# Kernel tuning notes

Hardware: AMD Instinct MI355X
Metric: run time of the kernel (lower is better)

The kernel has to match this reference:

```python
import jax, jax.numpy as jnp
import numpy as np

V, B, T, D, H, HS, L, F = 50257, 16, 256, 64, 4, 16, 4, 256
EPS = 1e-5


def layernorm(x, g, b):
    mu = jnp.mean(x, axis=-1, keepdims=True)
    var = jnp.var(x, axis=-1, keepdims=True)
    return (x - mu) * jax.lax.rsqrt(var + EPS) * g + b


def setup_inputs() -> dict:
    key = jax.random.key(0)
    ks = jax.random.split(key, 20)
    s = 0.02
    inp = {
        "idx": jax.random.randint(ks[0], (B, T), 0, V),
        "targets": jax.random.randint(ks[1], (B, T), 0, V),
        "tok_emb": jax.random.normal(ks[2], (V, D), jnp.float32) * s,
        "pos_emb": jax.random.normal(ks[3], (T, D), jnp.float32) * s,
        "Wq": jax.random.normal(ks[4], (L, H, D, HS), jnp.float32) * s,
        "Wk": jax.random.normal(ks[5], (L, H, D, HS), jnp.float32) * s,
        "Wv": jax.random.normal(ks[6], (L, H, D, HS), jnp.float32) * s,
        "Wo": jax.random.normal(ks[7], (L, D, D), jnp.float32) * s,
        "bo": jnp.zeros((L, D), jnp.float32),
        "ln1_g": jnp.ones((L, D), jnp.float32),
        "ln1_b": jnp.zeros((L, D), jnp.float32),
        "ln2_g": jnp.ones((L, D), jnp.float32),
        "ln2_b": jnp.zeros((L, D), jnp.float32),
        "W1": jax.random.normal(ks[8], (L, D, F), jnp.float32) * s,
        "b1": jnp.zeros((L, F), jnp.float32),
        "W2": jax.random.normal(ks[9], (L, F, D), jnp.float32) * s,
        "b2": jnp.zeros((L, D), jnp.float32),
        "lnf_g": jnp.ones((D,), jnp.float32),
        "lnf_b": jnp.zeros((D,), jnp.float32),
        "Whead": jax.random.normal(ks[10], (D, V), jnp.float32) * s,
        "bhead": jnp.zeros((V,), jnp.float32),
    }
    return inp


def reference(idx, targets, tok_emb, pos_emb, Wq, Wk, Wv, Wo, bo,
              ln1_g, ln1_b, ln2_g, ln2_b, W1, b1, W2, b2,
              lnf_g, lnf_b, Whead, bhead):
    Tt = idx.shape[1]
    x = tok_emb[idx] + pos_emb[:Tt]  # [B,T,D]
    causal = jnp.tril(jnp.ones((Tt, Tt), bool))
    for l in range(L):
        h = layernorm(x, ln1_g[l], ln1_b[l])
        q = jnp.einsum('btd,hds->bhts', h, Wq[l])
        k = jnp.einsum('btd,hds->bhts', h, Wk[l])
        v = jnp.einsum('btd,hds->bhts', h, Wv[l])
        # NOTE: original applies NO 1/sqrt(head_size) scaling
        scores = jnp.einsum('bhts,bhus->bhtu', q, k)  # [B,H,T,T]
        scores = jnp.where(causal, scores, -jnp.inf)
        attn = jax.nn.softmax(scores, axis=-1)
        o = jnp.einsum('bhtu,bhus->bths', attn, v)  # [B,T,H,HS]
        o = o.reshape(o.shape[0], Tt, D)
        x = x + o @ Wo[l] + bo[l]
        h2 = layernorm(x, ln2_g[l], ln2_b[l])
        x = x + jax.nn.relu(h2 @ W1[l] + b1[l]) @ W2[l] + b2[l]
    x = layernorm(x, lnf_g, lnf_b)
    logits = x @ Whead + bhead  # [B,T,V]
    logp = jax.nn.log_softmax(logits, axis=-1)
    loss = -jnp.mean(jnp.take_along_axis(logp, targets[..., None], axis=-1))
    return (logits, loss)
```

## Files before the change

### kernel.cpp

```cpp
#include <hip/hip_runtime.h>
#include <hip/hip_bf16.h>
#include <math.h>

constexpr int NV  = 50257;
constexpr int NB  = 16;
constexpr int NT  = 256;
constexpr int ND  = 64;
constexpr int NH  = 4;
constexpr int NHS = 16;
constexpr int NL  = 4;
constexpr int NF  = 256;
constexpr int NN  = NB * NT;
constexpr float EPS = 1e-5f;

constexpr int NCB2 = 200;
constexpr int NVP  = NCB2 * 256;
constexpr int LOGITS = NN * NV;
constexpr int RB_N  = NN / 64;
constexpr int CB_PER_XCD = NCB2 / 8;

constexpr int X_OFF   = 0;
constexpr int Q_OFF   = X_OFF  + NN * ND;
constexpr int K_OFF   = Q_OFF  + NN * ND;
constexpr int V_OFF   = K_OFF  + NN * ND;
constexpr int O_OFF   = V_OFF  + NN * ND;
constexpr int A_OFF   = O_OFF  + NN * ND;
constexpr int XFB_OFF = A_OFF  + NN * NF;
constexpr int WM_OFF  = XFB_OFF + NN * ND / 2;
constexpr int WS2_OFF = WM_OFF + NCB2 * NN;
constexpr int WHB_OFF = WS2_OFF + NCB2 * NN;
constexpr int LP_OFF  = WHB_OFF + NVP * 32;

typedef __bf16 bf16x8 __attribute__((ext_vector_type(8)));
typedef float  f32x4  __attribute__((ext_vector_type(4)));

__global__ __launch_bounds__(256) void k_ln_qkv(
        float* __restrict__ x, const float* __restrict__ g, const float* __restrict__ bb,
        const float* __restrict__ Wq, const float* __restrict__ Wk, const float* __restrict__ Wv,
        float* __restrict__ q, float* __restrict__ k, float* __restrict__ v,
        const int* __restrict__ idx, const float* __restrict__ tok,
        const float* __restrict__ pos, int first) {
    __shared__ float hs[16][65];
    int t = threadIdx.x;
    int r0 = blockIdx.x * 16;
    if (first) {
        for (int i = t; i < 16 * 64; i += 256) {
            int n = r0 + (i >> 6);
            int tt = n & (NT - 1), d = i & 63;
            float e = tok[idx[n] * ND + d] + pos[tt * ND + d];
            hs[i >> 6][i & 63] = e;
            x[(size_t)r0 * 64 + i] = e;
        }
    } else {
        for (int i = t; i < 16 * 64; i += 256)
            hs[i >> 6][i & 63] = x[r0 * 64 + i];
    }
    __syncthreads();
    {
        int row = t >> 4, sub = t & 15;
        float s = 0.f, s2 = 0.f;
        #pragma unroll
        for (int j = 0; j < 4; j++) { float vv = hs[row][sub * 4 + j]; s += vv; s2 += vv * vv; }
        #pragma unroll
        for (int off = 1; off < 16; off <<= 1) { s += __shfl_xor(s, off); s2 += __shfl_xor(s2, off); }
        float mu = s * (1.f / 64.f);
        float var = s2 * (1.f / 64.f) - mu * mu;
        float rs = rsqrtf(var + EPS);
        #pragma unroll
        for (int j = 0; j < 4; j++) {
            int d = sub * 4 + j;
            hs[row][d] = (hs[row][d] - mu) * rs * g[d] + bb[d];
        }
    }
    __syncthreads();
    int c = t & 63, rg = t >> 6;
    int head = c >> 4, sidx = c & 15;
    float aq[4], ak[4], av[4];
    #pragma unroll
    for (int i = 0; i < 4; i++) { aq[i] = 0.f; ak[i] = 0.f; av[i] = 0.f; }
    for (int kk = 0; kk < 64; kk++) {
        float wq = Wq[(head * 64 + kk) * 16 + sidx];
        float wk = Wk[(head * 64 + kk) * 16 + sidx];
        float wv = Wv[(head * 64 + kk) * 16 + sidx];
        #pragma unroll
        for (int i = 0; i < 4; i++) {
            float h = hs[rg * 4 + i][kk];
            aq[i] += h * wq; ak[i] += h * wk; av[i] += h * wv;
        }
    }
    #pragma unroll
    for (int i = 0; i < 4; i++) {
        int n = r0 + rg * 4 + i;
        int b = n >> 8, tt = n & 255;
        int oidx = ((b * NH + head) * NT + tt) * NHS + sidx;
        q[oidx] = aq[i]; k[oidx] = ak[i]; v[oidx] = av[i];
    }
}

__global__ __launch_bounds__(256) void k_attn(
        const float* __restrict__ q, const float* __restrict__ k,
        const float* __restrict__ v, float* __restrict__ o) {
    __shared__ float ks[256][16];
    __shared__ float vs[256][16];
    int blk = blockIdx.x;
    int bh = blk >> 2;
    int tq = blk & 3;
    int t = threadIdx.x;
    int tl = t >> 2, sub = t & 3;
    int tt = tq * 64 + tl;
    int nrows = tq * 64 + 64;
    const float* kb = k + bh * NT * NHS;
    const float* vb = v + bh * NT * NHS;
    for (int i = t; i < nrows * 16; i += 256) {
        (&ks[0][0])[i] = kb[i];
        (&vs[0][0])[i] = vb[i];
    }
    __syncthreads();
    float qr[16];
    const float* qp = q + bh * NT * NHS + tt * NHS;
    #pragma unroll
    for (int j = 0; j < 16; j += 4) {
        float4 qv = *(const float4*)(qp + j);
        qr[j] = qv.x; qr[j+1] = qv.y; qr[j+2] = qv.z; qr[j+3] = qv.w;
    }
    float m = -1e30f, l = 0.f, acc[16];
    #pragma unroll
    for (int j = 0; j < 16; j++) acc[j] = 0.f;
    for (int u = sub; u <= tt; u += 4) {
        float s = 0.f;
        #pragma unroll
        for (int j = 0; j < 16; j++) s += qr[j] * ks[u][j];
        float mn = fmaxf(m, s);
        float corr = __expf(m - mn);
        float p = __expf(s - mn);
        l = l * corr + p;
        #pragma unroll
        for (int j = 0; j < 16; j++) acc[j] = acc[j] * corr + p * vs[u][j];
        m = mn;
    }
    #pragma unroll
    for (int off = 1; off < 4; off <<= 1) {
        float mo = __shfl_xor(m, off);
        float lo = __shfl_xor(l, off);
        float mn = fmaxf(m, mo);
        float c1 = __expf(m - mn), c2 = __expf(mo - mn);
        l = l * c1 + lo * c2;
        #pragma unroll
        for (int j = 0; j < 16; j++) {
            float ao = __shfl_xor(acc[j], off);
            acc[j] = acc[j] * c1 + ao * c2;
        }
        m = mn;
    }
    float inv = 1.f / l;
    int b = bh >> 2, h = bh & 3;
    float* op = o + (b * NT + tt) * ND + h * NHS;
    float o0, o1, o2, o3;
    if (sub == 0)      { o0 = acc[0];  o1 = acc[1];  o2 = acc[2];  o3 = acc[3];  }
    else if (sub == 1) { o0 = acc[4];  o1 = acc[5];  o2 = acc[6];  o3 = acc[7];  }
    else if (sub == 2) { o0 = acc[8];  o1 = acc[9];  o2 = acc[10]; o3 = acc[11]; }
    else               { o0 = acc[12]; o1 = acc[13]; o2 = acc[14]; o3 = acc[15]; }
    float4 ov = make_float4(o0 * inv, o1 * inv, o2 * inv, o3 * inv);
    *(float4*)(op + sub * 4) = ov;
}

__global__ __launch_bounds__(256) void k_post(
        const float* __restrict__ o, const float* __restrict__ Wo, const float* __restrict__ bo,
        const float* __restrict__ g2, const float* __restrict__ bg2,
        const float* __restrict__ W1, const float* __restrict__ b1,
        const float* __restrict__ W2, const float* __restrict__ b2m,
        float* __restrict__ x,
        const float* __restrict__ lg, const float* __restrict__ lb,
        __hip_bfloat16* __restrict__ xfb, int last) {
    __shared__ float os[16][65];
    __shared__ float xs[16][65];
    __shared__ float as[16][257];
    int t = threadIdx.x;
    int r0 = blockIdx.x * 16;
    for (int i = t; i < 16 * 64; i += 256)
        os[i >> 6][i & 63] = o[r0 * 64 + i];
    __syncthreads();
    int c = t & 63, rg = t >> 6;
    {
        float pr[4] = {0.f, 0.f, 0.f, 0.f};
        for (int kk = 0; kk < 64; kk++) {
            float w = Wo[kk * 64 + c];
            #pragma unroll
            for (int i = 0; i < 4; i++) pr[i] += os[rg * 4 + i][kk] * w;
        }
        float bias = bo[c];
        #pragma unroll
        for (int i = 0; i < 4; i++) {
            int row = rg * 4 + i;
            xs[row][c] = x[(r0 + row) * 64 + c] + pr[i] + bias;
        }
    }
    __syncthreads();
    {
        int row = t >> 4, sub = t & 15;
        float s = 0.f, s2 = 0.f;
        #pragma unroll
        for (int j = 0; j < 4; j++) { float vv = xs[row][sub * 4 + j]; s += vv; s2 += vv * vv; }
        #pragma unroll
        for (int off = 1; off < 16; off <<= 1) { s += __shfl_xor(s, off); s2 += __shfl_xor(s2, off); }
        float mu = s * (1.f / 64.f);
        float var = s2 * (1.f / 64.f) - mu * mu;
        float rs = rsqrtf(var + EPS);
        #pragma unroll
        for (int j = 0; j < 4; j++) {
            int d = sub * 4 + j;
            os[row][d] = (xs[row][d] - mu) * rs * g2[d] + bg2[d];
        }
    }
    __syncthreads();
    {
        float m1[16];
        #pragma unroll
        for (int i = 0; i < 16; i++) m1[i] = 0.f;
        for (int kk = 0; kk < 64; kk++) {
            float w = W1[kk * NF + t];
            #pragma unroll
            for (int i = 0; i < 16; i++) m1[i] += os[i][kk] * w;
        }
        float bb1 = b1[t];
        #pragma unroll
        for (int i = 0; i < 16; i++) as[i][t] = fmaxf(m1[i] + bb1, 0.f);
    }
    __syncthreads();
    {
        float m2[4] = {0.f, 0.f, 0.f, 0.f};
        for (int kk = 0; kk < 256; kk++) {
            float w = W2[kk * 64 + c];
            #pragma unroll
            for (int i = 0; i < 4; i++) m2[i] += as[rg * 4 + i][kk] * w;
        }
        float bias = b2m[c];
        if (!last) {
            #pragma unroll
            for (int i = 0; i < 4; i++) {
                int row = rg * 4 + i;
                x[(r0 + row) * 64 + c] = xs[row][c] + m2[i] + bias;
            }
        } else {
            #pragma unroll
            for (int i = 0; i < 4; i++) {
                int row = rg * 4 + i;
                os[row][c] = xs[row][c] + m2[i] + bias;
            }
            __syncthreads();
            int row = t >> 4, sub = t & 15;
            float s = 0.f, s2 = 0.f;
            #pragma unroll
            for (int j = 0; j < 4; j++) { float vv = os[row][sub * 4 + j]; s += vv; s2 += vv * vv; }
            #pragma unroll
            for (int off = 1; off < 16; off <<= 1) { s += __shfl_xor(s, off); s2 += __shfl_xor(s2, off); }
            float mu = s * (1.f / 64.f);
            float var = s2 * (1.f / 64.f) - mu * mu;
            float rs = rsqrtf(var + EPS);
            #pragma unroll
            for (int j = 0; j < 4; j++) {
                int d = sub * 4 + j;
                float val = (os[row][d] - mu) * rs * lg[d] + lb[d];
                xfb[(r0 + row) * 64 + d] = __float2bfloat16(val);
            }
        }
    }
}

__global__ __launch_bounds__(256) void k_convW(
        const float* __restrict__ Wh, __hip_bfloat16* __restrict__ whb) {
    __shared__ float w[64][65];
    int t = threadIdx.x;
    int n0 = blockIdx.x * 64;
    for (int i = t; i < 64 * 64; i += 256) {
        int k = i >> 6, c = i & 63;
        int n = n0 + c;
        w[k][c] = (n < NV) ? Wh[k * NV + n] : 0.f;
    }
    __syncthreads();
    int c = t >> 2, kq = t & 3;
    int n = n0 + c;
    union { __hip_bfloat16 h[16]; uint4 u[2]; } pk;
    #pragma unroll
    for (int j = 0; j < 16; j++)
        pk.h[j] = __float2bfloat16(w[kq * 16 + j][c]);
    uint4* dst = (uint4*)(whb + (size_t)n * 64 + kq * 16);
    dst[0] = pk.u[0];
    dst[1] = pk.u[1];
}

__global__ __launch_bounds__(256) void k_head(
        const __hip_bfloat16* __restrict__ xfb, const __hip_bfloat16* __restrict__ whb,
        const float* __restrict__ bhead, float* __restrict__ out,
        float* __restrict__ wsum) {
    __shared__ float ssm[4][64];

    int i0 = blockIdx.x;
    int xcd = i0 & 7;
    int j  = i0 >> 3;
    int rb = j / CB_PER_XCD;
    int cb = xcd * CB_PER_XCD + (j - rb * CB_PER_XCD);

    int t = threadIdx.x;
    int w = t >> 6, l = t & 63;
    int lr = l & 15, lg = l >> 4;
    int r0 = rb * 64;
    int cw = cb * 256 + w * 64;
    int c4 = cw + lr * 4;

    bf16x8 a[4][2], b[4][2];
    {
        const __hip_bfloat16* ap = xfb + (size_t)(r0 + lr) * 64 + lg * 8;
        #pragma unroll
        for (int m = 0; m < 4; m++)
            #pragma unroll
            for (int ks = 0; ks < 2; ks++)
                a[m][ks] = *reinterpret_cast<const bf16x8*>(ap + m * 16 * 64 + ks * 32);
        const __hip_bfloat16* bp = whb + (size_t)c4 * 64 + lg * 8;
        #pragma unroll
        for (int n = 0; n < 4; n++)
            #pragma unroll
            for (int ks = 0; ks < 2; ks++)
                b[n][ks] = *reinterpret_cast<const bf16x8*>(bp + n * 64 + ks * 32);
    }

    f32x4 acc[4][4];
    #pragma unroll
    for (int m = 0; m < 4; m++)
        #pragma unroll
        for (int n = 0; n < 4; n++)
            #pragma unroll
            for (int j2 = 0; j2 < 4; j2++) acc[m][n][j2] = 0.f;

    #pragma unroll
    for (int ks = 0; ks < 2; ks++)
        #pragma unroll
        for (int m = 0; m < 4; m++)
            #pragma unroll
            for (int n = 0; n < 4; n++)
                acc[m][n] = __builtin_amdgcn_mfma_f32_16x16x32_bf16(a[m][ks], b[n][ks], acc[m][n], 0, 0, 0);

    bool all4 = (c4 + 3 < NV);
    float bias[4];
    bool  cok[4];
    if (all4) {
        float4 bv = *(const float4*)(bhead + c4);
        bias[0] = bv.x; bias[1] = bv.y; bias[2] = bv.z; bias[3] = bv.w;
        cok[0] = cok[1] = cok[2] = cok[3] = true;
    } else {
        #pragma unroll
        for (int n = 0; n < 4; n++) {
            int gc = c4 + n;
            cok[n] = (gc < NV);
            bias[n] = cok[n] ? bhead[gc] : 0.f;
        }
    }

    #pragma unroll
    for (int m = 0; m < 4; m++) {
        #pragma unroll
        for (int i = 0; i < 4; i++) {
            int rl = 4 * lg + i;
            int grow = r0 + m * 16 + rl;
            float vals[4];
            float es = 0.f;
            #pragma unroll
            for (int n = 0; n < 4; n++) {
                float v = acc[m][n][i] + bias[n];
                vals[n] = v;
                if (cok[n]) es += __expf(v);
            }
            #pragma unroll
            for (int off = 1; off < 16; off <<= 1) es += __shfl_xor(es, off);
            if (lr == 0) ssm[w][m * 16 + rl] = es;
            float* dst = out + (size_t)grow * NV + c4;
            if (all4) {
                float4 vv = make_float4(vals[0], vals[1], vals[2], vals[3]);
                *(float4*)dst = vv;
            } else {
                #pragma unroll
                for (int n = 0; n < 4; n++)
                    if (cok[n]) dst[n] = vals[n];
            }
        }
    }

    __syncthreads();
    if (t < 64)
        wsum[cb * NN + r0 + t] = ssm[0][t] + ssm[1][t] + ssm[2][t] + ssm[3][t];
}

__global__ void k_loss1(const float* __restrict__ wsum,
                        const float* __restrict__ out, const int* __restrict__ targets,
                        float* __restrict__ lp) {
    int row = blockIdx.x * blockDim.x + threadIdx.x;
    if (row >= NN) return;
    float S = 0.f;
    for (int cb = 0; cb < NCB2; cb++)
        S += wsum[cb * NN + row];
    float lse = logf(S);
    int tg = targets[row];
    float lt = out[(size_t)row * NV + tg];
    lp[row] = lt - lse;
}

__global__ void k_loss2(const float* __restrict__ lp, float* __restrict__ out) {
    __shared__ float red[4];
    int t = threadIdx.x;
    float s = 0.f;
    for (int i = t; i < NN; i += 256) s += lp[i];
    for (int off = 1; off < 64; off <<= 1) s += __shfl_xor(s, off);
    if ((t & 63) == 0) red[t >> 6] = s;
    __syncthreads();
    if (t == 0) {
        float tot = red[0] + red[1] + red[2] + red[3];
        out[LOGITS] = -tot / (float)NN;
    }
}

extern "C" void kernel_launch(void* const* d_in, const int* in_sizes, int n_in,
                              void* d_out, int out_size, void* d_ws, size_t ws_size,
                              hipStream_t stream) {
    const int*   idx     = (const int*)d_in[0];
    const int*   targets = (const int*)d_in[1];
    const float* tok     = (const float*)d_in[2];
    const float* pos     = (const float*)d_in[3];
    const float* Wq      = (const float*)d_in[4];
    const float* Wk      = (const float*)d_in[5];
    const float* Wv      = (const float*)d_in[6];
    const float* Wo      = (const float*)d_in[7];
    const float* bo      = (const float*)d_in[8];
    const float* ln1g    = (const float*)d_in[9];
    const float* ln1b    = (const float*)d_in[10];
    const float* ln2g    = (const float*)d_in[11];
    const float* ln2b    = (const float*)d_in[12];
    const float* W1      = (const float*)d_in[13];
    const float* b1      = (const float*)d_in[14];
    const float* W2      = (const float*)d_in[15];
    const float* b2      = (const float*)d_in[16];
    const float* lnfg    = (const float*)d_in[17];
    const float* lnfb    = (const float*)d_in[18];
    const float* Wh      = (const float*)d_in[19];
    const float* bhead   = (const float*)d_in[20];

    float* ws = (float*)d_ws;
    float* x  = ws + X_OFF;
    float* q  = ws + Q_OFF;
    float* k  = ws + K_OFF;
    float* v  = ws + V_OFF;
    float* o  = ws + O_OFF;
    __hip_bfloat16* xfb = (__hip_bfloat16*)(ws + XFB_OFF);
    float* wsm = ws + WS2_OFF;
    __hip_bfloat16* whb = (__hip_bfloat16*)(ws + WHB_OFF);
    float* lp  = ws + LP_OFF;
    float* out = (float*)d_out;

    k_convW<<<NVP / 64, 256, 0, stream>>>(Wh, whb);

    for (int l = 0; l < NL; l++) {
        k_ln_qkv<<<NN / 16, 256, 0, stream>>>(x, ln1g + l * ND, ln1b + l * ND,
                                              Wq + l * NH * ND * NHS, Wk + l * NH * ND * NHS,
                                              Wv + l * NH * ND * NHS, q, k, v,
                                              idx, tok, pos, (l == 0) ? 1 : 0);
        k_attn<<<NB * NH * 4, 256, 0, stream>>>(q, k, v, o);
        k_post<<<NN / 16, 256, 0, stream>>>(o, Wo + l * ND * ND, bo + l * ND,
                                            ln2g + l * ND, ln2b + l * ND,
                                            W1 + l * ND * NF, b1 + l * NF,
                                            W2 + l * NF * ND, b2 + l * ND, x,
                                            lnfg, lnfb, xfb, (l == NL - 1) ? 1 : 0);
    }

    k_head<<<NCB2 * RB_N, 256, 0, stream>>>(xfb, whb, bhead, out, wsm);

    k_loss1<<<NN / 256, 256, 0, stream>>>(wsm, out, targets, lp);
    k_loss2<<<1, 256, 0, stream>>>(lp, out);
}
```

Before: 525.2 us.

## Fuse next-layer LN1+QKV into post kernel; nontemporal logits stores

Computes the next layer's LayerNorm and Q/K/V projection at the end of k_post, so three k_ln_qkv launches and their re-read of x are removed; the first layer still uses a standalone embedding+LN+QKV kernel. The head kernel now writes logits with nontemporal stores and moves the row-sum shuffle reductions after all stores, so the large logits write stream bypasses cache and does not interleave with cross-lane reductions. In exchange, k_post becomes longer, needs more registers and one more barrier, and the q/k/v layout has to match what k_attn expects.

```diff
diff --git a/kernel.cpp b/kernel.cpp
--- a/kernel.cpp
+++ b/kernel.cpp
@@ -39,21 +39,16 @@
         const float* __restrict__ Wq, const float* __restrict__ Wk, const float* __restrict__ Wv,
         float* __restrict__ q, float* __restrict__ k, float* __restrict__ v,
         const int* __restrict__ idx, const float* __restrict__ tok,
-        const float* __restrict__ pos, int first) {
+        const float* __restrict__ pos) {
     __shared__ float hs[16][65];
     int t = threadIdx.x;
     int r0 = blockIdx.x * 16;
-    if (first) {
-        for (int i = t; i < 16 * 64; i += 256) {
-            int n = r0 + (i >> 6);
-            int tt = n & (NT - 1), d = i & 63;
-            float e = tok[idx[n] * ND + d] + pos[tt * ND + d];
-            hs[i >> 6][i & 63] = e;
-            x[(size_t)r0 * 64 + i] = e;
-        }
-    } else {
-        for (int i = t; i < 16 * 64; i += 256)
-            hs[i >> 6][i & 63] = x[r0 * 64 + i];
+    for (int i = t; i < 16 * 64; i += 256) {
+        int n = r0 + (i >> 6);
+        int tt = n & (NT - 1), d = i & 63;
+        float e = tok[idx[n] * ND + d] + pos[tt * ND + d];
+        hs[i >> 6][i & 63] = e;
+        x[(size_t)r0 * 64 + i] = e;
     }
     __syncthreads();
     {
@@ -170,6 +165,10 @@
         const float* __restrict__ W1, const float* __restrict__ b1,
         const float* __restrict__ W2, const float* __restrict__ b2m,
         float* __restrict__ x,
+        const float* __restrict__ g1n, const float* __restrict__ b1n,
+        const float* __restrict__ Wqn, const float* __restrict__ Wkn,
+        const float* __restrict__ Wvn,
+        float* __restrict__ q, float* __restrict__ k, float* __restrict__ v,
         const float* __restrict__ lg, const float* __restrict__ lb,
         __hip_bfloat16* __restrict__ xfb, int last) {
     __shared__ float os[16][65];
@@ -235,34 +234,78 @@
             for (int i = 0; i < 4; i++) m2[i] += as[rg * 4 + i][kk] * w;
         }
         float bias = b2m[c];
-        if (!last) {
+        #pragma unroll
+        for (int i = 0; i < 4; i++) {
+            int row = rg * 4 + i;
+            xs[row][c] += m2[i] + bias;
+        }
+    }
+    __syncthreads();
+
+    if (last) {
+        int row = t >> 4, sub = t & 15;
+        float s = 0.f, s2 = 0.f;
+        #pragma unroll
+        for (int j = 0; j < 4; j++) { float vv = xs[row][sub * 4 + j]; s += vv; s2 += vv * vv; }
+        #pragma unroll
+        for (int off = 1; off < 16; off <<= 1) { s += __shfl_xor(s, off); s2 += __shfl_xor(s2, off); }
+        float mu = s * (1.f / 64.f);
+        float var = s2 * (1.f / 64.f) - mu * mu;
+        float rs = rsqrtf(var + EPS);
+        #pragma unroll
+        for (int j = 0; j < 4; j++) {
+            int d = sub * 4 + j;
+            float val = (xs[row][d] - mu) * rs * lg[d] + lb[d];
+            xfb[(r0 + row) * 64 + d] = __float2bfloat16(val);
+        }
+        return;
+    }
+
+    {
+        #pragma unroll
+        for (int i = 0; i < 4; i++) {
+            int row = rg * 4 + i;
+            x[(r0 + row) * 64 + c] = xs[row][c];
+        }
+    }
+    {
+        int row = t >> 4, sub = t & 15;
+        float s = 0.f, s2 = 0.f;
+        #pragma unroll
+        for (int j = 0; j < 4; j++) { float vv = xs[row][sub * 4 + j]; s += vv; s2 += vv * vv; }
+        #pragma unroll
+        for (int off = 1; off < 16; off <<= 1) { s += __shfl_xor(s, off); s2 += __shfl_xor(s2, off); }
+        float mu = s * (1.f / 64.f);
+        float var = s2 * (1.f / 64.f) - mu * mu;
+        float rs = rsqrtf(var + EPS);
+        #pragma unroll
+        for (int j = 0; j < 4; j++) {
+            int d = sub * 4 + j;
+            os[row][d] = (xs[row][d] - mu) * rs * g1n[d] + b1n[d];
+        }
+    }
+    __syncthreads();
+    {
+        int head = c >> 4, sidx = c & 15;
+        float aq[4], ak[4], av[4];
+        #pragma unroll
+        for (int i = 0; i < 4; i++) { aq[i] = 0.f; ak[i] = 0.f; av[i] = 0.f; }
+        for (int kk = 0; kk < 64; kk++) {
+            float wq = Wqn[(head * 64 + kk) * 16 + sidx];
+            float wk = Wkn[(head * 64 + kk) * 16 + sidx];
+            float wv = Wvn[(head * 64 + kk) * 16 + sidx];
             #pragma unroll
             for (int i = 0; i < 4; i++) {
-                int row = rg * 4 + i;
-                x[(r0 + row) * 64 + c] = xs[row][c] + m2[i] + bias;
+                float h = os[rg * 4 + i][kk];
+                aq[i] += h * wq; ak[i] += h * wk; av[i] += h * wv;
             }
-        } else {
-            #pragma unroll
-            for (int i = 0; i < 4; i++) {
-                int row = rg * 4 + i;
-                os[row][c] = xs[row][c] + m2[i] + bias;
-            }
-            __syncthreads();
-            int row = t >> 4, sub = t & 15;
-            float s = 0.f, s2 = 0.f;
-            #pragma unroll
-            for (int j = 0; j < 4; j++) { float vv = os[row][sub * 4 + j]; s += vv; s2 += vv * vv; }
-            #pragma unroll
-            for (int off = 1; off < 16; off <<= 1) { s += __shfl_xor(s, off); s2 += __shfl_xor(s2, off); }
-            float mu = s * (1.f / 64.f);
-            float var = s2 * (1.f / 64.f) - mu * mu;
-            float rs = rsqrtf(var + EPS);
-            #pragma unroll
-            for (int j = 0; j < 4; j++) {
-                int d = sub * 4 + j;
-                float val = (os[row][d] - mu) * rs * lg[d] + lb[d];
-                xfb[(r0 + row) * 64 + d] = __float2bfloat16(val);
-            }
+        }
+        #pragma unroll
+        for (int i = 0; i < 4; i++) {
+            int n = r0 + rg * 4 + i;
+            int b = n >> 8, tt = n & 255;
+            int oidx = ((b * NH + head) * NT + tt) * NHS + sidx;
+            q[oidx] = aq[i]; k[oidx] = ak[i]; v[oidx] = av[i];
         }
     }
 }
@@ -356,6 +399,7 @@
         }
     }
 
+    float es[16];
     #pragma unroll
     for (int m = 0; m < 4; m++) {
         #pragma unroll
@@ -363,25 +407,34 @@
             int rl = 4 * lg + i;
             int grow = r0 + m * 16 + rl;
             float vals[4];
-            float es = 0.f;
+            float e = 0.f;
             #pragma unroll
             for (int n = 0; n < 4; n++) {
                 float v = acc[m][n][i] + bias[n];
                 vals[n] = v;
-                if (cok[n]) es += __expf(v);
+                if (cok[n]) e += __expf(v);
             }
-            #pragma unroll
-            for (int off = 1; off < 16; off <<= 1) es += __shfl_xor(es, off);
-            if (lr == 0) ssm[w][m * 16 + rl] = es;
+            es[m * 4 + i] = e;
             float* dst = out + (size_t)grow * NV + c4;
             if (all4) {
-                float4 vv = make_float4(vals[0], vals[1], vals[2], vals[3]);
-                *(float4*)dst = vv;
+                f32x4 vv = {vals[0], vals[1], vals[2], vals[3]};
+                __builtin_nontemporal_store(vv, (f32x4*)dst);
             } else {
                 #pragma unroll
                 for (int n = 0; n < 4; n++)
-                    if (cok[n]) dst[n] = vals[n];
+                    if (cok[n]) __builtin_nontemporal_store(vals[n], dst + n);
             }
+        }
+    }
+
+    #pragma unroll
+    for (int m = 0; m < 4; m++) {
+        #pragma unroll
+        for (int i = 0; i < 4; i++) {
+            float e = es[m * 4 + i];
+            #pragma unroll
+            for (int off = 1; off < 16; off <<= 1) e += __shfl_xor(e, off);
+            if (lr == 0) ssm[w][m * 16 + 4 * lg + i] = e;
         }
     }
 
@@ -457,17 +510,23 @@
 
     k_convW<<<NVP / 64, 256, 0, stream>>>(Wh, whb);
 
+    k_ln_qkv<<<NN / 16, 256, 0, stream>>>(x, ln1g, ln1b, Wq, Wk, Wv, q, k, v,
+                                          idx, tok, pos);
+
     for (int l = 0; l < NL; l++) {
-        k_ln_qkv<<<NN / 16, 256, 0, stream>>>(x, ln1g + l * ND, ln1b + l * ND,
-                                              Wq + l * NH * ND * NHS, Wk + l * NH * ND * NHS,
-                                              Wv + l * NH * ND * NHS, q, k, v,
-                                              idx, tok, pos, (l == 0) ? 1 : 0);
+        int last = (l == NL - 1) ? 1 : 0;
+        int ln = last ? l : l + 1;
         k_attn<<<NB * NH * 4, 256, 0, stream>>>(q, k, v, o);
         k_post<<<NN / 16, 256, 0, stream>>>(o, Wo + l * ND * ND, bo + l * ND,
                                             ln2g + l * ND, ln2b + l * ND,
                                             W1 + l * ND * NF, b1 + l * NF,
                                             W2 + l * NF * ND, b2 + l * ND, x,
-                                            lnfg, lnfb, xfb, (l == NL - 1) ? 1 : 0);
+                                            ln1g + ln * ND, ln1b + ln * ND,
+                                            Wq + ln * NH * ND * NHS,
+                                            Wk + ln * NH * ND * NHS,
+                                            Wv + ln * NH * ND * NHS,
+                                            q, k, v,
+                                            lnfg, lnfb, xfb, last);
     }
 
     k_head<<<NCB2 * RB_N, 256, 0, stream>>>(xfb, whb, bhead, out, wsm);
```

New measurement: 525.8 us. Within noise of the previous version (+0.1%).
